# Optimization experiments

Measured on AMD Instinct MI355X. Metric: run time of the kernel, lower is better.

The kernel has to match this reference:

```python
import jax, jax.numpy as jnp
import numpy as np

N_NODES = 100000
N_EDGES = 3200000
IN_DIM = 62
OUT_DIM = 16
EDGE_DIM = 2


def setup_inputs() -> dict:
    key = jax.random.key(0)
    ks = jax.random.split(key, 8)
    h = jax.random.normal(ks[0], (N_NODES, IN_DIM), dtype=jnp.float32)
    e = jax.random.normal(ks[1], (N_EDGES, EDGE_DIM), dtype=jnp.float32)
    src = jax.random.randint(ks[2], (N_EDGES,), 0, N_NODES, dtype=jnp.int32)
    dst = jax.random.randint(ks[3], (N_EDGES,), 0, N_NODES, dtype=jnp.int32)
    # xavier-normal-ish scaled weights
    W_fc = jax.random.normal(ks[4], (OUT_DIM, IN_DIM), dtype=jnp.float32) * 0.2
    W_attn = jax.random.normal(ks[5], (1, 2 * OUT_DIM + EDGE_DIM), dtype=jnp.float32) * 0.2
    W_edge = jax.random.normal(ks[6], (EDGE_DIM, EDGE_DIM), dtype=jnp.float32) * 0.5
    W_e2n = jax.random.normal(ks[7], (OUT_DIM, EDGE_DIM), dtype=jnp.float32) * 0.5
    return {"h": h, "e": e, "src": src, "dst": dst, "W_fc": W_fc,
            "W_attn": W_attn, "W_edge": W_edge, "W_e2n": W_e2n}


def _agat_forward(h, e, src, dst, W_fc, W_attn, W_edge, W_e2n):
    n = h.shape[0]
    d = W_fc.shape[0]
    z = h @ W_fc.T                      # [N, D]
    ex = e @ W_edge.T                   # [E, edge_dim]
    # attn_fc([z_src, z_dst, ex]) split into per-part projections
    Wa_src = W_attn[:, :d]              # [1, D]
    Wa_dst = W_attn[:, d:2 * d]         # [1, D]
    Wa_e = W_attn[:, 2 * d:]            # [1, edge_dim]
    a_src = (z @ Wa_src.T)[:, 0]        # [N] per-node, gathered per-edge
    a_dst = (z @ Wa_dst.T)[:, 0]        # [N]
    a = a_src[src] + a_dst[dst] + (ex @ Wa_e.T)[:, 0]   # [E]
    e_att = jax.nn.leaky_relu(a, negative_slope=0.01)    # [E]
    # segment softmax over incoming edges of each dst node
    m = jax.ops.segment_max(e_att, dst, num_segments=n)  # [N]
    w = jnp.exp(e_att - m[dst])                           # [E]
    denom = jax.ops.segment_sum(w, dst, num_segments=n)   # [N]
    attn = w / denom[dst]                                  # [E]
    # message = z_src + ez; aggregated as attn-weighted sum (matches
    # sum(attn*z) + sum(attn*ez) in reduce_func)
    ez = ex @ W_e2n.T                                      # [E, D]
    msg = attn[:, None] * (z[src] + ez)                    # [E, D]
    return jax.ops.segment_sum(msg, dst, num_segments=n)   # [N, D]


def reference(h, e, src, dst, W_fc, W_attn, W_edge, W_e2n):
    return _agat_forward(h, e, src, dst, W_fc, W_attn, W_edge, W_e2n)
```

## Files before the change

### kernel.cpp

```cpp
#include <hip/hip_runtime.h>
#include <hip/hip_fp16.h>

#define N_NODES 100000
#define N_EDGES 3200000
#define IN_DIM  62
#define OUT_DIM 16

#define EBC    6144
#define EPT    (EBC / 1024)
#define NEB    ((N_EDGES + EBC - 1) / EBC)
#define NPB    ((N_NODES + 1023) / 1024)
#define NBUCK  ((N_NODES + 63) / 64)
#define CAPL   4096
#define CSTR   16

typedef int nat_i2 __attribute__((ext_vector_type(2)));

__global__ __launch_bounds__(1024) void proj_append_kernel(
    const float* __restrict__ h,
    const float* __restrict__ W_fc,
    const float* __restrict__ W_attn,
    const float* __restrict__ e,
    const int*   __restrict__ src,
    const int*   __restrict__ dst,
    __half* __restrict__ zh,
    float* __restrict__ a_src_arr,
    float* __restrict__ a_dst_arr,
    int*   __restrict__ cursor,
    nat_i2* __restrict__ records,
    int cap)
{
    __shared__ int  cnt[NBUCK];
    __shared__ int  pfx[NBUCK];
    __shared__ int  combo[NBUCK];
    __shared__ int2 pay[EBC];
    __shared__ unsigned short pbkt[EBC];
    __shared__ int  wsum[16];

    int tid = threadIdx.x;

    if (blockIdx.x < NPB) {
        int i = blockIdx.x * 1024 + tid;
        if (i >= N_NODES) return;

        float acc[OUT_DIM];
#pragma unroll
        for (int j = 0; j < OUT_DIM; ++j) acc[j] = 0.f;

        const float2* __restrict__ hr = (const float2*)(h + (size_t)i * IN_DIM);
#pragma unroll
        for (int kk = 0; kk < IN_DIM / 2; ++kk) {
            float2 hv = hr[kk];
#pragma unroll
            for (int j = 0; j < OUT_DIM; ++j) {
                acc[j] += hv.x * W_fc[j * IN_DIM + 2 * kk]
                        + hv.y * W_fc[j * IN_DIM + 2 * kk + 1];
            }
        }

        float asrc = 0.f, adst = 0.f;
#pragma unroll
        for (int j = 0; j < OUT_DIM; ++j) {
            asrc += acc[j] * W_attn[j];
            adst += acc[j] * W_attn[OUT_DIM + j];
        }

        union { __half hx[16]; uint4 q[2]; } u;
#pragma unroll
        for (int j = 0; j < OUT_DIM; ++j) u.hx[j] = __float2half(acc[j]);
        uint4* __restrict__ zrow = (uint4*)(zh + (size_t)i * OUT_DIM);
        zrow[0] = u.q[0];
        zrow[1] = u.q[1];

        a_src_arr[i] = asrc;
        a_dst_arr[i] = adst;
        return;
    }

    int be = blockIdx.x - NPB;
    long ebase = (long)be * EBC;
    int chunk_n = (int)min((long)EBC, (long)N_EDGES - ebase);

    int dv[EPT], sv[EPT];
    float2 ev[EPT];
#pragma unroll
    for (int j = 0; j < EPT; ++j) {
        int p = tid + j * 1024;
        dv[j] = -1;
        if (p < chunk_n) {
            long eid = ebase + p;
            dv[j] = dst[eid];
            sv[j] = src[eid];
            ev[j] = ((const float2*)e)[eid];
        }
    }

    for (int t = tid; t < NBUCK; t += 1024) cnt[t] = 0;
    __syncthreads();

#pragma unroll
    for (int j = 0; j < EPT; ++j)
        if (dv[j] >= 0) atomicAdd(&cnt[dv[j] >> 6], 1);
    __syncthreads();

    int b0 = 2 * tid, b1 = b0 + 1;
    int c0 = (b0 < NBUCK) ? cnt[b0] : 0;
    int c1 = (b1 < NBUCK) ? cnt[b1] : 0;
    if (b0 < NBUCK) cnt[b0] = 0;
    if (b1 < NBUCK) cnt[b1] = 0;
    int gb0 = 0, gb1 = 0;
    if (c0) gb0 = atomicAdd(&cursor[b0 * CSTR], c0);
    if (c1) gb1 = atomicAdd(&cursor[b1 * CSTR], c1);

    int ts = c0 + c1;
    {
        int lane = tid & 63, wid = tid >> 6;
        int x = ts;
#pragma unroll
        for (int off = 1; off < 64; off <<= 1) {
            int y = __shfl_up(x, off, 64);
            if (lane >= off) x += y;
        }
        if (lane == 63) wsum[wid] = x;
        __syncthreads();
        if (wid == 0) {
            int v = (lane < 16) ? wsum[lane] : 0;
#pragma unroll
            for (int off = 1; off < 16; off <<= 1) {
                int y = __shfl_up(v, off, 64);
                if (lane >= off) v += y;
            }
            if (lane < 16) wsum[lane] = v;
        }
        __syncthreads();
        int texcl = x - ts + (wid ? wsum[wid - 1] : 0);
        if (b0 < NBUCK) { pfx[b0] = texcl;      combo[b0] = b0 * cap + gb0 - texcl; }
        if (b1 < NBUCK) { pfx[b1] = texcl + c0; combo[b1] = b1 * cap + gb1 - (texcl + c0); }
    }
    __syncthreads();

#pragma unroll
    for (int j = 0; j < EPT; ++j) {
        if (dv[j] >= 0) {
            int b = dv[j] >> 6;
            union { __half2 h2; int i; } uu;
            uu.h2.x = __float2half(ev[j].x);
            uu.h2.y = __float2half(ev[j].y);
            int r = atomicAdd(&cnt[b], 1);
            int q = pfx[b] + r;
            pay[q]  = make_int2(uu.i, sv[j] | ((dv[j] & 63) << 17));
            pbkt[q] = (unsigned short)b;
        }
    }
    __syncthreads();

    for (int p = tid; p < chunk_n; p += 1024) {
        int2 v = pay[p];
        int bb = pbkt[p];
        int pos = combo[bb] + p;
        if (pos < (bb + 1) * cap) {
            nat_i2 vv; vv.x = v.x; vv.y = v.y;
            __builtin_nontemporal_store(vv, records + pos);
        }
    }
}

__global__ __launch_bounds__(1024) void bucket_gather_kernel(
    const int*    __restrict__ cursor,
    const nat_i2* __restrict__ records,
    const __half* __restrict__ zh,
    const float*  __restrict__ a_src_arr,
    const float*  __restrict__ a_dst_arr,
    const float*  __restrict__ W_attn,
    const float*  __restrict__ W_edge,
    const float*  __restrict__ W_e2n,
    float* __restrict__ out, int cap)
{
    __shared__ int2 rec[CAPL];
    __shared__ unsigned short inv[CAPL];
    __shared__ unsigned int exb[CAPL];
    __shared__ int hist[64], pfx[64], cur[64];
    __shared__ float adst_l[64];

    int b   = blockIdx.x;
    int tid = threadIdx.x;
    long lo = (long)b * cap;
    int n   = cursor[b * CSTR];
    int nl  = n < cap ? n : cap;
    if (nl > CAPL) nl = CAPL;

    if (tid < 64) {
        hist[tid] = 0; cur[tid] = 0;
        int node = (b << 6) + tid;
        adst_l[tid] = (node < N_NODES) ? a_dst_arr[node] : 0.f;
    }
    __syncthreads();

    float we00 = W_edge[0], we01 = W_edge[1], we10 = W_edge[2], we11 = W_edge[3];
    float wa0  = W_attn[2 * OUT_DIM], wa1 = W_attn[2 * OUT_DIM + 1];

    int ld0 = -1, ld1 = -1, ld2 = -1, ld3 = -1;
#define EDGEW(J, LD)                                                        \
    {                                                                       \
        int k = tid + (J) * 1024;                                           \
        if (k < nl) {                                                       \
            nat_i2 r = __builtin_nontemporal_load(records + lo + k);        \
            int s  = r.y & 0x1FFFF;                                         \
            LD     = (r.y >> 17) & 63;                                      \
            union { int i; __half2 h2; } ue; ue.i = r.x;                    \
            float e0 = __low2float(ue.h2), e1 = __high2float(ue.h2);        \
            float ex0 = e0 * we00 + e1 * we01;                              \
            float ex1 = e0 * we10 + e1 * we11;                              \
            float a = a_src_arr[s] + adst_l[LD] + ex0 * wa0 + ex1 * wa1;    \
            float ea = (a > 0.f) ? a : 0.01f * a;                           \
            float w  = __expf(ea);                                          \
            rec[k] = make_int2(__float_as_int(w), r.y);                     \
            union { unsigned int i; __half2 h2; } up;                       \
            up.h2.x = __float2half(ex0);                                    \
            up.h2.y = __float2half(ex1);                                    \
            exb[k] = up.i;                                                  \
            atomicAdd(&hist[LD], 1);                                        \
        }                                                                   \
    }
    EDGEW(0, ld0) EDGEW(1, ld1) EDGEW(2, ld2) EDGEW(3, ld3)
#undef EDGEW
    __syncthreads();

    if (tid < 64) pfx[tid] = hist[tid];
    __syncthreads();
    for (int off = 1; off < 64; off <<= 1) {
        int t = 0;
        if (tid < 64 && tid >= off) t = pfx[tid - off];
        __syncthreads();
        if (tid < 64) pfx[tid] += t;
        __syncthreads();
    }
    if (tid < 64) pfx[tid] -= hist[tid];
    __syncthreads();

#define INVW(J, LD)                                                         \
    if (LD >= 0) {                                                          \
        int k = tid + (J) * 1024;                                           \
        int r = atomicAdd(&cur[LD], 1);                                     \
        inv[pfx[LD] + r] = (unsigned short)k;                               \
    }
    INVW(0, ld0) INVW(1, ld1) INVW(2, ld2) INVW(3, ld3)
#undef INVW
    __syncthreads();

    int ld   = tid >> 4;
    int lane = tid & 15;
    int node = (b << 6) + ld;
    if (node >= N_NODES) return;

    int m    = hist[ld];
    int base = pfx[ld];

    float acc0 = 0.f, acc1 = 0.f, accw0 = 0.f, accw1 = 0.f;
    float ax00 = 0.f, ax01 = 0.f, ax10 = 0.f, ax11 = 0.f;

    int i = 0;
    for (; i + 1 < m; i += 2) {
        int k0 = inv[base + i];
        int k1 = inv[base + i + 1];
        int2 r0 = rec[k0];
        int2 r1 = rec[k1];
        float w0 = __int_as_float(r0.x);
        float w1 = __int_as_float(r1.x);
        int s0 = r0.y & 0x1FFFF;
        int s1 = r1.y & 0x1FFFF;
        union { unsigned int i; __half2 h2; } x0, x1;
        x0.i = exb[k0];
        x1.i = exb[k1];

        float zv0 = __half2float(zh[s0 * OUT_DIM + lane]);
        float zv1 = __half2float(zh[s1 * OUT_DIM + lane]);

        acc0  += w0 * zv0;                 acc1  += w1 * zv1;
        accw0 += w0;                       accw1 += w1;
        ax00  += w0 * __low2float(x0.h2);  ax01  += w1 * __low2float(x1.h2);
        ax10  += w0 * __high2float(x0.h2); ax11  += w1 * __high2float(x1.h2);
    }
    if (i < m) {
        int k0 = inv[base + i];
        int2 r0 = rec[k0];
        float w0 = __int_as_float(r0.x);
        int s0 = r0.y & 0x1FFFF;
        union { unsigned int i; __half2 h2; } x0;
        x0.i = exb[k0];
        float zv0 = __half2float(zh[s0 * OUT_DIM + lane]);
        acc0  += w0 * zv0;
        accw0 += w0;
        ax00  += w0 * __low2float(x0.h2);
        ax10  += w0 * __high2float(x0.h2);
    }

    float acc  = acc0 + acc1;
    float accw = accw0 + accw1;
    float ax0  = ax00 + ax01;
    float ax1  = ax10 + ax11;

    float ez   = ax0 * W_e2n[2 * lane] + ax1 * W_e2n[2 * lane + 1];
    float invw = (accw != 0.f) ? (1.f / accw) : 0.f;
    out[(size_t)node * OUT_DIM + lane] = (acc + ez) * invw;
}


__global__ __launch_bounds__(256) void node_proj_fb_kernel(
    const float* __restrict__ h,
    const float* __restrict__ W_fc,
    const float* __restrict__ W_attn,
    float* __restrict__ z,
    float* __restrict__ a_src_arr,
    float* __restrict__ a_dst_arr,
    float* __restrict__ denom,
    float* __restrict__ out)
{
    int i = blockIdx.x * blockDim.x + threadIdx.x;
    if (i >= N_NODES) return;

    float acc[OUT_DIM];
#pragma unroll
    for (int j = 0; j < OUT_DIM; ++j) acc[j] = 0.f;

    const float2* __restrict__ hr = (const float2*)(h + (size_t)i * IN_DIM);
#pragma unroll
    for (int kk = 0; kk < IN_DIM / 2; ++kk) {
        float2 hv = hr[kk];
#pragma unroll
        for (int j = 0; j < OUT_DIM; ++j) {
            acc[j] += hv.x * W_fc[j * IN_DIM + 2 * kk]
                    + hv.y * W_fc[j * IN_DIM + 2 * kk + 1];
        }
    }

    float asrc = 0.f, adst = 0.f;
#pragma unroll
    for (int j = 0; j < OUT_DIM; ++j) {
        asrc += acc[j] * W_attn[j];
        adst += acc[j] * W_attn[OUT_DIM + j];
    }

    float4* __restrict__ zrow = (float4*)(z + (size_t)i * OUT_DIM);
    zrow[0] = make_float4(acc[0],  acc[1],  acc[2],  acc[3]);
    zrow[1] = make_float4(acc[4],  acc[5],  acc[6],  acc[7]);
    zrow[2] = make_float4(acc[8],  acc[9],  acc[10], acc[11]);
    zrow[3] = make_float4(acc[12], acc[13], acc[14], acc[15]);

    a_src_arr[i] = asrc;
    a_dst_arr[i] = adst;
    denom[i] = 0.f;

    float4 z4 = make_float4(0.f, 0.f, 0.f, 0.f);
    float4* __restrict__ orow = (float4*)(out + (size_t)i * OUT_DIM);
    orow[0] = z4; orow[1] = z4; orow[2] = z4; orow[3] = z4;
}

__global__ __launch_bounds__(256) void edge_kernel(
    const float* __restrict__ e,
    const int*   __restrict__ src,
    const int*   __restrict__ dst,
    const float* __restrict__ W_attn,
    const float* __restrict__ W_edge,
    const float* __restrict__ W_e2n,
    const float* __restrict__ z,
    const float* __restrict__ a_src_arr,
    const float* __restrict__ a_dst_arr,
    float* __restrict__ denom,
    float* __restrict__ out)
{
    int eid = blockIdx.x * blockDim.x + threadIdx.x;
    if (eid >= N_EDGES) return;

    int s = src[eid];
    int d = dst[eid];

    float2 ev = ((const float2*)e)[eid];
    float ex0 = ev.x * W_edge[0] + ev.y * W_edge[1];
    float ex1 = ev.x * W_edge[2] + ev.y * W_edge[3];

    float a = a_src_arr[s] + a_dst_arr[d]
            + ex0 * W_attn[2 * OUT_DIM] + ex1 * W_attn[2 * OUT_DIM + 1];
    float ea = (a > 0.f) ? a : 0.01f * a;
    float w  = __expf(ea);

    unsafeAtomicAdd(denom + d, w);

    const float4* __restrict__ zrow = (const float4*)(z + (size_t)s * OUT_DIM);
    float4 z0 = zrow[0], z1 = zrow[1], z2 = zrow[2], z3 = zrow[3];

    float* __restrict__ orow = out + (size_t)d * OUT_DIM;
    float zs[OUT_DIM] = { z0.x, z0.y, z0.z, z0.w,
                          z1.x, z1.y, z1.z, z1.w,
                          z2.x, z2.y, z2.z, z2.w,
                          z3.x, z3.y, z3.z, z3.w };
#pragma unroll
    for (int j = 0; j < OUT_DIM; ++j) {
        float ez = ex0 * W_e2n[2 * j] + ex1 * W_e2n[2 * j + 1];
        unsafeAtomicAdd(orow + j, w * (zs[j] + ez));
    }
}

__global__ __launch_bounds__(256) void normalize_kernel(
    float* __restrict__ out, const float* __restrict__ denom)
{
    int tid = blockIdx.x * blockDim.x + threadIdx.x;
    const int total = N_NODES * OUT_DIM / 4;
    if (tid >= total) return;
    int n = tid >> 2;
    float dn = denom[n];
    float inv = (dn != 0.f) ? (1.f / dn) : 0.f;
    float4 v = ((float4*)out)[tid];
    v.x *= inv; v.y *= inv; v.z *= inv; v.w *= inv;
    ((float4*)out)[tid] = v;
}

extern "C" void kernel_launch(void* const* d_in, const int* in_sizes, int n_in,
                              void* d_out, int out_size, void* d_ws, size_t ws_size,
                              hipStream_t stream)
{
    const float* h      = (const float*)d_in[0];
    const float* e      = (const float*)d_in[1];
    const int*   src    = (const int*)  d_in[2];
    const int*   dst    = (const int*)  d_in[3];
    const float* W_fc   = (const float*)d_in[4];
    const float* W_attn = (const float*)d_in[5];
    const float* W_edge = (const float*)d_in[6];
    const float* W_e2n  = (const float*)d_in[7];
    float* out = (float*)d_out;

    char* ws = (char*)d_ws;

    size_t off = 0;
    __half* zh        = (__half*)(ws + off); off += (size_t)N_NODES * OUT_DIM * 2;
    float*  a_src_arr = (float*) (ws + off); off += (size_t)N_NODES * 4;
    float*  a_dst_arr = (float*) (ws + off); off += (size_t)N_NODES * 4;
    int*    cursor    = (int*)   (ws + off); off += (size_t)NBUCK * CSTR * 4;
    size_t rec_off = (off + 255) & ~(size_t)255;

    int cap = 0;
    if      (ws_size >= rec_off + (size_t)NBUCK * 4096 * 8) cap = 4096;
    else if (ws_size >= rec_off + (size_t)NBUCK * 3072 * 8) cap = 3072;
    else if (ws_size >= rec_off + (size_t)NBUCK * 2560 * 8) cap = 2560;
    else if (ws_size >= rec_off + (size_t)NBUCK * 2304 * 8) cap = 2304;

    if (cap) {
        nat_i2* records = (nat_i2*)(ws + rec_off);

        hipMemsetAsync(cursor, 0, (size_t)NBUCK * CSTR * sizeof(int), stream);

        proj_append_kernel<<<NPB + NEB, 1024, 0, stream>>>(
            h, W_fc, W_attn, e, src, dst,
            zh, a_src_arr, a_dst_arr, cursor, records, cap);

        bucket_gather_kernel<<<NBUCK, 1024, 0, stream>>>(
            cursor, records, zh, a_src_arr, a_dst_arr,
            W_attn, W_edge, W_e2n, out, cap);
    } else {
        size_t foff = 0;
        float* z     = (float*)(ws + foff); foff += (size_t)N_NODES * OUT_DIM * 4;
        float* asrc  = (float*)(ws + foff); foff += (size_t)N_NODES * 4;
        float* adst  = (float*)(ws + foff); foff += (size_t)N_NODES * 4;
        float* denom = (float*)(ws + foff); foff += (size_t)N_NODES * 4;

        node_proj_fb_kernel<<<(N_NODES + 255) / 256, 256, 0, stream>>>(
            h, W_fc, W_attn, z, asrc, adst, denom, out);

        edge_kernel<<<(N_EDGES + 255) / 256, 256, 0, stream>>>(
            e, src, dst, W_attn, W_edge, W_e2n, z, asrc, adst, denom, out);

        normalize_kernel<<<(N_NODES * OUT_DIM / 4 + 255) / 256, 256, 0, stream>>>(
            out, denom);
    }
}
```

Before: 220.5 us.

## Use 256-node buckets with chunked two-block gather and atomic partial accumulation

Buckets grow from 64 to 256 destination nodes, and each bucket's record segment is padded to a multiple of 8 with zero-weight sentinel records. This is meant to give aligned, fuller writes and fewer cursor atomics. The gather kernel now runs two 512-thread blocks per bucket. They walk 2048-record chunks alternately, compute per-node partial numerators and denominators with 4 lanes per node using 8-byte loads of z, and add them atomically into zeroed global buffers. A separate normalize kernel then divides. This removes the fixed per-bucket shared-memory capacity, but adds atomics, an extra pass, and a larger memset.

```diff
diff --git a/kernel.cpp b/kernel.cpp
--- a/kernel.cpp
+++ b/kernel.cpp
@@ -6,13 +6,17 @@
 #define IN_DIM  62
 #define OUT_DIM 16
 
-#define EBC    6144
-#define EPT    (EBC / 1024)
+#define EBC    4096
+#define EPT    4
 #define NEB    ((N_EDGES + EBC - 1) / EBC)
 #define NPB    ((N_NODES + 1023) / 1024)
-#define NBUCK  ((N_NODES + 63) / 64)
-#define CAPL   4096
+#define BSH    8
+#define BNODES 256
+#define NB2    ((N_NODES + BNODES - 1) / BNODES)
+#define PCAP   6912
+#define CHK    2048
 #define CSTR   16
+#define PADY   ((int)0x82000000u)
 
 typedef int nat_i2 __attribute__((ext_vector_type(2)));
 
@@ -30,12 +34,13 @@
     nat_i2* __restrict__ records,
     int cap)
 {
-    __shared__ int  cnt[NBUCK];
-    __shared__ int  pfx[NBUCK];
-    __shared__ int  combo[NBUCK];
-    __shared__ int2 pay[EBC];
-    __shared__ unsigned short pbkt[EBC];
+    __shared__ int  cnt[NB2];
+    __shared__ int  pfx[NB2];
+    __shared__ int  combo[NB2];
+    __shared__ int2 pay[PCAP];
+    __shared__ unsigned short pbkt[PCAP];
     __shared__ int  wsum[16];
+    __shared__ int  sh_ptot;
 
     int tid = threadIdx.x;
 
@@ -95,27 +100,26 @@
         }
     }
 
-    for (int t = tid; t < NBUCK; t += 1024) cnt[t] = 0;
+    for (int t = tid; t < NB2; t += 1024) cnt[t] = 0;
     __syncthreads();
 
 #pragma unroll
     for (int j = 0; j < EPT; ++j)
-        if (dv[j] >= 0) atomicAdd(&cnt[dv[j] >> 6], 1);
+        if (dv[j] >= 0) atomicAdd(&cnt[dv[j] >> BSH], 1);
     __syncthreads();
 
-    int b0 = 2 * tid, b1 = b0 + 1;
-    int c0 = (b0 < NBUCK) ? cnt[b0] : 0;
-    int c1 = (b1 < NBUCK) ? cnt[b1] : 0;
-    if (b0 < NBUCK) cnt[b0] = 0;
-    if (b1 < NBUCK) cnt[b1] = 0;
-    int gb0 = 0, gb1 = 0;
-    if (c0) gb0 = atomicAdd(&cursor[b0 * CSTR], c0);
-    if (c1) gb1 = atomicAdd(&cursor[b1 * CSTR], c1);
-
-    int ts = c0 + c1;
+    int c = 0, n8 = 0, gb = 0;
+    if (tid < NB2) {
+        c  = cnt[tid];
+        n8 = (c + 7) & ~7;
+        cnt[tid] = 0;
+        if (n8) gb = atomicAdd(&cursor[tid * CSTR], n8);
+    }
+
+    int texcl;
     {
         int lane = tid & 63, wid = tid >> 6;
-        int x = ts;
+        int x = n8;
 #pragma unroll
         for (int off = 1; off < 64; off <<= 1) {
             int y = __shfl_up(x, off, 64);
@@ -133,30 +137,38 @@
             if (lane < 16) wsum[lane] = v;
         }
         __syncthreads();
-        int texcl = x - ts + (wid ? wsum[wid - 1] : 0);
-        if (b0 < NBUCK) { pfx[b0] = texcl;      combo[b0] = b0 * cap + gb0 - texcl; }
-        if (b1 < NBUCK) { pfx[b1] = texcl + c0; combo[b1] = b1 * cap + gb1 - (texcl + c0); }
-    }
+        texcl = x - n8 + (wid ? wsum[wid - 1] : 0);
+    }
+
+    if (tid < NB2) {
+        pfx[tid]   = texcl;
+        combo[tid] = tid * cap + gb - texcl;
+        for (int q = texcl; q < texcl + n8; ++q) {
+            pay[q]  = make_int2(0, PADY);
+            pbkt[q] = (unsigned short)tid;
+        }
+    }
+    if (tid == NB2 - 1) sh_ptot = texcl + n8;
     __syncthreads();
 
 #pragma unroll
     for (int j = 0; j < EPT; ++j) {
         if (dv[j] >= 0) {
-            int b = dv[j] >> 6;
+            int b = dv[j] >> BSH;
             union { __half2 h2; int i; } uu;
             uu.h2.x = __float2half(ev[j].x);
             uu.h2.y = __float2half(ev[j].y);
             int r = atomicAdd(&cnt[b], 1);
             int q = pfx[b] + r;
-            pay[q]  = make_int2(uu.i, sv[j] | ((dv[j] & 63) << 17));
-            pbkt[q] = (unsigned short)b;
+            pay[q] = make_int2(uu.i, sv[j] | ((dv[j] & (BNODES - 1)) << 17));
         }
     }
     __syncthreads();
 
-    for (int p = tid; p < chunk_n; p += 1024) {
-        int2 v = pay[p];
-        int bb = pbkt[p];
+    int ptot = sh_ptot;
+    for (int p = tid; p < ptot; p += 1024) {
+        int2 v  = pay[p];
+        int  bb = pbkt[p];
         int pos = combo[bb] + p;
         if (pos < (bb + 1) * cap) {
             nat_i2 vv; vv.x = v.x; vv.y = v.y;
@@ -165,7 +177,7 @@
     }
 }
 
-__global__ __launch_bounds__(1024) void bucket_gather_kernel(
+__global__ __launch_bounds__(512) void bucket_gather_kernel(
     const int*    __restrict__ cursor,
     const nat_i2* __restrict__ records,
     const __half* __restrict__ zh,
@@ -174,24 +186,26 @@
     const float*  __restrict__ W_attn,
     const float*  __restrict__ W_edge,
     const float*  __restrict__ W_e2n,
-    float* __restrict__ out, int cap)
-{
-    __shared__ int2 rec[CAPL];
-    __shared__ unsigned short inv[CAPL];
-    __shared__ unsigned int exb[CAPL];
-    __shared__ int hist[64], pfx[64], cur[64];
-    __shared__ float adst_l[64];
-
-    int b   = blockIdx.x;
+    float* __restrict__ num,
+    float* __restrict__ den,
+    int cap)
+{
+    __shared__ int2 rec[CHK];
+    __shared__ unsigned int exb[CHK];
+    __shared__ unsigned short inv[CHK];
+    __shared__ int hist[257], pfxs[257], cur[257];
+    __shared__ float adst_l[BNODES];
+    __shared__ int wsum4[4];
+
+    int b   = blockIdx.x >> 1;
+    int hb  = blockIdx.x & 1;
     int tid = threadIdx.x;
     long lo = (long)b * cap;
     int n   = cursor[b * CSTR];
-    int nl  = n < cap ? n : cap;
-    if (nl > CAPL) nl = CAPL;
-
-    if (tid < 64) {
-        hist[tid] = 0; cur[tid] = 0;
-        int node = (b << 6) + tid;
+    if (n > cap) n = cap;
+
+    if (tid < BNODES) {
+        int node = b * BNODES + tid;
         adst_l[tid] = (node < N_NODES) ? a_dst_arr[node] : 0.f;
     }
     __syncthreads();
@@ -199,110 +213,138 @@
     float we00 = W_edge[0], we01 = W_edge[1], we10 = W_edge[2], we11 = W_edge[3];
     float wa0  = W_attn[2 * OUT_DIM], wa1 = W_attn[2 * OUT_DIM + 1];
 
-    int ld0 = -1, ld1 = -1, ld2 = -1, ld3 = -1;
+    int lane4 = (tid & 3) * 4;
+
+    float aA[2][4], aW[2], aX0[2], aX1[2];
+#pragma unroll
+    for (int sp = 0; sp < 2; ++sp) {
+        aW[sp] = 0.f; aX0[sp] = 0.f; aX1[sp] = 0.f;
+#pragma unroll
+        for (int f = 0; f < 4; ++f) aA[sp][f] = 0.f;
+    }
+
+    for (int cb = hb * CHK; cb < n; cb += 2 * CHK) {
+        int cn = n - cb; if (cn > CHK) cn = CHK;
+
+        __syncthreads();
+        if (tid < 257) { hist[tid] = 0; cur[tid] = 0; }
+        __syncthreads();
+
+        int ld0 = -1, ld1 = -1, ld2 = -1, ld3 = -1;
 #define EDGEW(J, LD)                                                        \
-    {                                                                       \
-        int k = tid + (J) * 1024;                                           \
-        if (k < nl) {                                                       \
-            nat_i2 r = __builtin_nontemporal_load(records + lo + k);        \
-            int s  = r.y & 0x1FFFF;                                         \
-            LD     = (r.y >> 17) & 63;                                      \
-            union { int i; __half2 h2; } ue; ue.i = r.x;                    \
-            float e0 = __low2float(ue.h2), e1 = __high2float(ue.h2);        \
-            float ex0 = e0 * we00 + e1 * we01;                              \
-            float ex1 = e0 * we10 + e1 * we11;                              \
-            float a = a_src_arr[s] + adst_l[LD] + ex0 * wa0 + ex1 * wa1;    \
-            float ea = (a > 0.f) ? a : 0.01f * a;                           \
-            float w  = __expf(ea);                                          \
-            rec[k] = make_int2(__float_as_int(w), r.y);                     \
-            union { unsigned int i; __half2 h2; } up;                       \
-            up.h2.x = __float2half(ex0);                                    \
-            up.h2.y = __float2half(ex1);                                    \
-            exb[k] = up.i;                                                  \
-            atomicAdd(&hist[LD], 1);                                        \
-        }                                                                   \
-    }
-    EDGEW(0, ld0) EDGEW(1, ld1) EDGEW(2, ld2) EDGEW(3, ld3)
+        {                                                                   \
+            int kk = tid + (J) * 512;                                       \
+            if (kk < cn) {                                                  \
+                nat_i2 r = __builtin_nontemporal_load(records + lo + cb + kk); \
+                int s = r.y & 0x1FFFF;                                      \
+                LD = (r.y >> 17) & 0x1FF;                  \
+                union { int i; __half2 h2; } ue; ue.i = r.x;                \
+                float e0 = __low2float(ue.h2), e1 = __high2float(ue.h2);    \
+                float ex0 = e0 * we00 + e1 * we01;                          \
+                float ex1 = e0 * we10 + e1 * we11;                          \
+                float a = a_src_arr[s] + adst_l[LD & 255] + ex0 * wa0 + ex1 * wa1; \
+                float ea = (a > 0.f) ? a : 0.01f * a;                       \
+                float w  = __expf(ea);                                      \
+                if (r.y < 0) w = 0.f;                       \
+                rec[kk] = make_int2(__float_as_int(w), r.y);                \
+                union { unsigned int i; __half2 h2; } up;                   \
+                up.h2.x = __float2half(ex0);                                \
+                up.h2.y = __float2half(ex1);                                \
+                exb[kk] = up.i;                                             \
+                atomicAdd(&hist[LD], 1);                                    \
+            }                                                               \
+        }
+        EDGEW(0, ld0) EDGEW(1, ld1) EDGEW(2, ld2) EDGEW(3, ld3)
 #undef EDGEW
-    __syncthreads();
-
-    if (tid < 64) pfx[tid] = hist[tid];
-    __syncthreads();
-    for (int off = 1; off < 64; off <<= 1) {
-        int t = 0;
-        if (tid < 64 && tid >= off) t = pfx[tid - off];
-        __syncthreads();
-        if (tid < 64) pfx[tid] += t;
-        __syncthreads();
-    }
-    if (tid < 64) pfx[tid] -= hist[tid];
-    __syncthreads();
+        __syncthreads();
+
+        int hh = 0, xx = 0;
+        int lane = tid & 63, wv = tid >> 6;
+        if (tid < 256) {
+            hh = hist[tid]; xx = hh;
+#pragma unroll
+            for (int off = 1; off < 64; off <<= 1) {
+                int y = __shfl_up(xx, off, 64);
+                if (lane >= off) xx += y;
+            }
+            if (lane == 63) wsum4[wv] = xx;
+        }
+        __syncthreads();
+        if (tid == 0) {
+            int rr = 0;
+#pragma unroll
+            for (int i2 = 0; i2 < 4; ++i2) { int t = wsum4[i2]; wsum4[i2] = rr; rr += t; }
+        }
+        __syncthreads();
+        if (tid < 256) {
+            pfxs[tid] = xx - hh + wsum4[wv];
+            if (tid == 255) pfxs[256] = xx + wsum4[3];
+        }
+        __syncthreads();
 
 #define INVW(J, LD)                                                         \
-    if (LD >= 0) {                                                          \
-        int k = tid + (J) * 1024;                                           \
-        int r = atomicAdd(&cur[LD], 1);                                     \
-        inv[pfx[LD] + r] = (unsigned short)k;                               \
-    }
-    INVW(0, ld0) INVW(1, ld1) INVW(2, ld2) INVW(3, ld3)
+        if (LD >= 0) {                                                      \
+            int kk = tid + (J) * 512;                                       \
+            int r = atomicAdd(&cur[LD], 1);                                 \
+            inv[pfxs[LD] + r] = (unsigned short)kk;                         \
+        }
+        INVW(0, ld0) INVW(1, ld1) INVW(2, ld2) INVW(3, ld3)
 #undef INVW
-    __syncthreads();
-
-    int ld   = tid >> 4;
-    int lane = tid & 15;
-    int node = (b << 6) + ld;
-    if (node >= N_NODES) return;
-
-    int m    = hist[ld];
-    int base = pfx[ld];
-
-    float acc0 = 0.f, acc1 = 0.f, accw0 = 0.f, accw1 = 0.f;
-    float ax00 = 0.f, ax01 = 0.f, ax10 = 0.f, ax11 = 0.f;
-
-    int i = 0;
-    for (; i + 1 < m; i += 2) {
-        int k0 = inv[base + i];
-        int k1 = inv[base + i + 1];
-        int2 r0 = rec[k0];
-        int2 r1 = rec[k1];
-        float w0 = __int_as_float(r0.x);
-        float w1 = __int_as_float(r1.x);
-        int s0 = r0.y & 0x1FFFF;
-        int s1 = r1.y & 0x1FFFF;
-        union { unsigned int i; __half2 h2; } x0, x1;
-        x0.i = exb[k0];
-        x1.i = exb[k1];
-
-        float zv0 = __half2float(zh[s0 * OUT_DIM + lane]);
-        float zv1 = __half2float(zh[s1 * OUT_DIM + lane]);
-
-        acc0  += w0 * zv0;                 acc1  += w1 * zv1;
-        accw0 += w0;                       accw1 += w1;
-        ax00  += w0 * __low2float(x0.h2);  ax01  += w1 * __low2float(x1.h2);
-        ax10  += w0 * __high2float(x0.h2); ax11  += w1 * __high2float(x1.h2);
-    }
-    if (i < m) {
-        int k0 = inv[base + i];
-        int2 r0 = rec[k0];
-        float w0 = __int_as_float(r0.x);
-        int s0 = r0.y & 0x1FFFF;
-        union { unsigned int i; __half2 h2; } x0;
-        x0.i = exb[k0];
-        float zv0 = __half2float(zh[s0 * OUT_DIM + lane]);
-        acc0  += w0 * zv0;
-        accw0 += w0;
-        ax00  += w0 * __low2float(x0.h2);
-        ax10  += w0 * __high2float(x0.h2);
-    }
-
-    float acc  = acc0 + acc1;
-    float accw = accw0 + accw1;
-    float ax0  = ax00 + ax01;
-    float ax1  = ax10 + ax11;
-
-    float ez   = ax0 * W_e2n[2 * lane] + ax1 * W_e2n[2 * lane + 1];
-    float invw = (accw != 0.f) ? (1.f / accw) : 0.f;
-    out[(size_t)node * OUT_DIM + lane] = (acc + ez) * invw;
+        __syncthreads();
+
+#pragma unroll
+        for (int sp = 0; sp < 2; ++sp) {
+            int nl_  = sp * 128 + (tid >> 2);
+            int m    = hist[nl_];
+            int base = pfxs[nl_];
+            for (int i = 0; i < m; ++i) {
+                int k = inv[base + i];
+                int2 r = rec[k];
+                float w = __int_as_float(r.x);
+                int s = r.y & 0x1FFFF;
+                unsigned int xe = exb[k];
+                uint2 zz = *(const uint2*)(zh + (size_t)s * OUT_DIM + lane4);
+                union { unsigned int i; __half2 h2; } za, zb, xu;
+                za.i = zz.x; zb.i = zz.y; xu.i = xe;
+                aA[sp][0] += w * __low2float(za.h2);
+                aA[sp][1] += w * __high2float(za.h2);
+                aA[sp][2] += w * __low2float(zb.h2);
+                aA[sp][3] += w * __high2float(zb.h2);
+                aW[sp]  += w;
+                aX0[sp] += w * __low2float(xu.h2);
+                aX1[sp] += w * __high2float(xu.h2);
+            }
+        }
+    }
+
+#pragma unroll
+    for (int sp = 0; sp < 2; ++sp) {
+        int node = b * BNODES + sp * 128 + (tid >> 2);
+        if (node < N_NODES) {
+#pragma unroll
+            for (int f = 0; f < 4; ++f) {
+                int j = lane4 + f;
+                float ez = aX0[sp] * W_e2n[2 * j] + aX1[sp] * W_e2n[2 * j + 1];
+                unsafeAtomicAdd(&num[(size_t)node * OUT_DIM + j], aA[sp][f] + ez);
+            }
+            if ((tid & 3) == 0) unsafeAtomicAdd(&den[node], aW[sp]);
+        }
+    }
+}
+
+__global__ __launch_bounds__(256) void normalize2_kernel(
+    const float* __restrict__ num, const float* __restrict__ den,
+    float* __restrict__ out)
+{
+    int t = blockIdx.x * blockDim.x + threadIdx.x;
+    const int total = N_NODES * OUT_DIM / 4;
+    if (t >= total) return;
+    int node = t >> 2;
+    float dn = den[node];
+    float iv = (dn != 0.f) ? (1.f / dn) : 0.f;
+    float4 v = ((const float4*)num)[t];
+    v.x *= iv; v.y *= iv; v.z *= iv; v.w *= iv;
+    ((float4*)out)[t] = v;
 }
 
 
@@ -435,27 +477,33 @@
     __half* zh        = (__half*)(ws + off); off += (size_t)N_NODES * OUT_DIM * 2;
     float*  a_src_arr = (float*) (ws + off); off += (size_t)N_NODES * 4;
     float*  a_dst_arr = (float*) (ws + off); off += (size_t)N_NODES * 4;
-    int*    cursor    = (int*)   (ws + off); off += (size_t)NBUCK * CSTR * 4;
+    off = (off + 255) & ~(size_t)255;
+    size_t mz_off = off;
+    int*    cursor = (int*)(ws + off);  off += ((size_t)NB2 * CSTR * 4 + 255) & ~(size_t)255;
+    float*  num    = (float*)(ws + off); off += (size_t)N_NODES * OUT_DIM * 4;
+    float*  den    = (float*)(ws + off); off += (size_t)N_NODES * 4;
+    size_t mz_bytes = off - mz_off;
     size_t rec_off = (off + 255) & ~(size_t)255;
 
     int cap = 0;
-    if      (ws_size >= rec_off + (size_t)NBUCK * 4096 * 8) cap = 4096;
-    else if (ws_size >= rec_off + (size_t)NBUCK * 3072 * 8) cap = 3072;
-    else if (ws_size >= rec_off + (size_t)NBUCK * 2560 * 8) cap = 2560;
-    else if (ws_size >= rec_off + (size_t)NBUCK * 2304 * 8) cap = 2304;
+    if      (ws_size >= rec_off + (size_t)NB2 * 12288 * 8) cap = 12288;
+    else if (ws_size >= rec_off + (size_t)NB2 * 11776 * 8) cap = 11776;
 
     if (cap) {
         nat_i2* records = (nat_i2*)(ws + rec_off);
 
-        hipMemsetAsync(cursor, 0, (size_t)NBUCK * CSTR * sizeof(int), stream);
+        hipMemsetAsync(ws + mz_off, 0, mz_bytes, stream);
 
         proj_append_kernel<<<NPB + NEB, 1024, 0, stream>>>(
             h, W_fc, W_attn, e, src, dst,
             zh, a_src_arr, a_dst_arr, cursor, records, cap);
 
-        bucket_gather_kernel<<<NBUCK, 1024, 0, stream>>>(
+        bucket_gather_kernel<<<2 * NB2, 512, 0, stream>>>(
             cursor, records, zh, a_src_arr, a_dst_arr,
-            W_attn, W_edge, W_e2n, out, cap);
+            W_attn, W_edge, W_e2n, num, den, cap);
+
+        normalize2_kernel<<<(N_NODES * OUT_DIM / 4 + 255) / 256, 256, 0, stream>>>(
+            num, den, out);
     } else {
         size_t foff = 0;
         float* z     = (float*)(ws + foff); foff += (size_t)N_NODES * OUT_DIM * 4;
```

After: 234.1 us. +6.2%, slower.

## Fuse projection, append and gather into one persistent cooperative kernel

Applied to the files above, without the earlier changes.

Replaces the memset plus two kernel launches with a single cooperative persistent kernel. It zeroes the cursors, runs the projection and append work units in a grid-stride loop, then the per-bucket gather, with grid-wide syncs between phases. Shared memory is a union of the two phase layouts, and the edge chunk shrinks from 6144 to 4096 so the persistent blocks fit. This removes launch gaps and kernel boundaries, but it adds grid-sync cost, limits the grid to one or two blocks per CU, and risks load imbalance.

```diff
diff --git a/kernel.cpp b/kernel.cpp
--- a/kernel.cpp
+++ b/kernel.cpp
@@ -1,83 +1,93 @@
 #include <hip/hip_runtime.h>
 #include <hip/hip_fp16.h>
+#include <hip/hip_cooperative_groups.h>
+
+namespace cg = cooperative_groups;
 
 #define N_NODES 100000
 #define N_EDGES 3200000
 #define IN_DIM  62
 #define OUT_DIM 16
 
-#define EBC    6144
-#define EPT    (EBC / 1024)
+#define EBC    4096
+#define EPT    4
 #define NEB    ((N_EDGES + EBC - 1) / EBC)
 #define NPB    ((N_NODES + 1023) / 1024)
 #define NBUCK  ((N_NODES + 63) / 64)
 #define CAPL   4096
 #define CSTR   16
+#define NCU    256
 
 typedef int nat_i2 __attribute__((ext_vector_type(2)));
 
-__global__ __launch_bounds__(1024) void proj_append_kernel(
-    const float* __restrict__ h,
-    const float* __restrict__ W_fc,
+struct AppendSh {
+    int  cnt[NBUCK];
+    int  pfx[NBUCK];
+    int  combo[NBUCK];
+    int2 pay[EBC];
+    unsigned short pbkt[EBC];
+    int  wsum[16];
+};
+struct GatherSh {
+    int2 rec[CAPL];
+    unsigned short inv[CAPL];
+    unsigned int exb[CAPL];
+    int hist[64], pfx[64], cur[64];
+    float adst_l[64];
+};
+union ShArena { AppendSh a; GatherSh g; };
+
+__device__ __forceinline__ void do_proj(
+    int u, int tid,
+    const float* __restrict__ h, const float* __restrict__ W_fc,
     const float* __restrict__ W_attn,
-    const float* __restrict__ e,
-    const int*   __restrict__ src,
-    const int*   __restrict__ dst,
-    __half* __restrict__ zh,
-    float* __restrict__ a_src_arr,
-    float* __restrict__ a_dst_arr,
-    int*   __restrict__ cursor,
-    nat_i2* __restrict__ records,
-    int cap)
-{
-    __shared__ int  cnt[NBUCK];
-    __shared__ int  pfx[NBUCK];
-    __shared__ int  combo[NBUCK];
-    __shared__ int2 pay[EBC];
-    __shared__ unsigned short pbkt[EBC];
-    __shared__ int  wsum[16];
-
-    int tid = threadIdx.x;
-
-    if (blockIdx.x < NPB) {
-        int i = blockIdx.x * 1024 + tid;
-        if (i >= N_NODES) return;
-
-        float acc[OUT_DIM];
-#pragma unroll
-        for (int j = 0; j < OUT_DIM; ++j) acc[j] = 0.f;
-
-        const float2* __restrict__ hr = (const float2*)(h + (size_t)i * IN_DIM);
-#pragma unroll
-        for (int kk = 0; kk < IN_DIM / 2; ++kk) {
-            float2 hv = hr[kk];
-#pragma unroll
-            for (int j = 0; j < OUT_DIM; ++j) {
-                acc[j] += hv.x * W_fc[j * IN_DIM + 2 * kk]
-                        + hv.y * W_fc[j * IN_DIM + 2 * kk + 1];
-            }
-        }
-
-        float asrc = 0.f, adst = 0.f;
+    __half* __restrict__ zh, float* __restrict__ a_src_arr,
+    float* __restrict__ a_dst_arr)
+{
+    int i = u * 1024 + tid;
+    if (i >= N_NODES) return;
+
+    float acc[OUT_DIM];
+#pragma unroll
+    for (int j = 0; j < OUT_DIM; ++j) acc[j] = 0.f;
+
+    const float2* __restrict__ hr = (const float2*)(h + (size_t)i * IN_DIM);
+#pragma unroll
+    for (int kk = 0; kk < IN_DIM / 2; ++kk) {
+        float2 hv = hr[kk];
 #pragma unroll
         for (int j = 0; j < OUT_DIM; ++j) {
-            asrc += acc[j] * W_attn[j];
-            adst += acc[j] * W_attn[OUT_DIM + j];
-        }
-
-        union { __half hx[16]; uint4 q[2]; } u;
-#pragma unroll
-        for (int j = 0; j < OUT_DIM; ++j) u.hx[j] = __float2half(acc[j]);
-        uint4* __restrict__ zrow = (uint4*)(zh + (size_t)i * OUT_DIM);
-        zrow[0] = u.q[0];
-        zrow[1] = u.q[1];
-
-        a_src_arr[i] = asrc;
-        a_dst_arr[i] = adst;
-        return;
-    }
-
-    int be = blockIdx.x - NPB;
+            acc[j] += hv.x * W_fc[j * IN_DIM + 2 * kk]
+                    + hv.y * W_fc[j * IN_DIM + 2 * kk + 1];
+        }
+    }
+
+    float asrc = 0.f, adst = 0.f;
+#pragma unroll
+    for (int j = 0; j < OUT_DIM; ++j) {
+        asrc += acc[j] * W_attn[j];
+        adst += acc[j] * W_attn[OUT_DIM + j];
+    }
+
+    union { __half hx[16]; uint4 q[2]; } uq;
+#pragma unroll
+    for (int j = 0; j < OUT_DIM; ++j) uq.hx[j] = __float2half(acc[j]);
+    uint4* __restrict__ zrow = (uint4*)(zh + (size_t)i * OUT_DIM);
+    zrow[0] = uq.q[0];
+    zrow[1] = uq.q[1];
+
+    a_src_arr[i] = asrc;
+    a_dst_arr[i] = adst;
+}
+
+__device__ __forceinline__ void do_append(
+    int be, int tid, AppendSh& S,
+    const float* __restrict__ e, const int* __restrict__ src,
+    const int* __restrict__ dst, int* __restrict__ cursor,
+    nat_i2* __restrict__ records, int cap)
+{
+    __syncthreads();
+
     long ebase = (long)be * EBC;
     int chunk_n = (int)min((long)EBC, (long)N_EDGES - ebase);
 
@@ -95,19 +105,19 @@
         }
     }
 
-    for (int t = tid; t < NBUCK; t += 1024) cnt[t] = 0;
+    for (int t = tid; t < NBUCK; t += 1024) S.cnt[t] = 0;
     __syncthreads();
 
 #pragma unroll
     for (int j = 0; j < EPT; ++j)
-        if (dv[j] >= 0) atomicAdd(&cnt[dv[j] >> 6], 1);
+        if (dv[j] >= 0) atomicAdd(&S.cnt[dv[j] >> 6], 1);
     __syncthreads();
 
     int b0 = 2 * tid, b1 = b0 + 1;
-    int c0 = (b0 < NBUCK) ? cnt[b0] : 0;
-    int c1 = (b1 < NBUCK) ? cnt[b1] : 0;
-    if (b0 < NBUCK) cnt[b0] = 0;
-    if (b1 < NBUCK) cnt[b1] = 0;
+    int c0 = (b0 < NBUCK) ? S.cnt[b0] : 0;
+    int c1 = (b1 < NBUCK) ? S.cnt[b1] : 0;
+    if (b0 < NBUCK) S.cnt[b0] = 0;
+    if (b1 < NBUCK) S.cnt[b1] = 0;
     int gb0 = 0, gb1 = 0;
     if (c0) gb0 = atomicAdd(&cursor[b0 * CSTR], c0);
     if (c1) gb1 = atomicAdd(&cursor[b1 * CSTR], c1);
@@ -121,21 +131,21 @@
             int y = __shfl_up(x, off, 64);
             if (lane >= off) x += y;
         }
-        if (lane == 63) wsum[wid] = x;
+        if (lane == 63) S.wsum[wid] = x;
         __syncthreads();
         if (wid == 0) {
-            int v = (lane < 16) ? wsum[lane] : 0;
+            int v = (lane < 16) ? S.wsum[lane] : 0;
 #pragma unroll
             for (int off = 1; off < 16; off <<= 1) {
                 int y = __shfl_up(v, off, 64);
                 if (lane >= off) v += y;
             }
-            if (lane < 16) wsum[lane] = v;
+            if (lane < 16) S.wsum[lane] = v;
         }
         __syncthreads();
-        int texcl = x - ts + (wid ? wsum[wid - 1] : 0);
-        if (b0 < NBUCK) { pfx[b0] = texcl;      combo[b0] = b0 * cap + gb0 - texcl; }
-        if (b1 < NBUCK) { pfx[b1] = texcl + c0; combo[b1] = b1 * cap + gb1 - (texcl + c0); }
+        int texcl = x - ts + (wid ? S.wsum[wid - 1] : 0);
+        if (b0 < NBUCK) { S.pfx[b0] = texcl;      S.combo[b0] = b0 * cap + gb0 - texcl; }
+        if (b1 < NBUCK) { S.pfx[b1] = texcl + c0; S.combo[b1] = b1 * cap + gb1 - (texcl + c0); }
     }
     __syncthreads();
 
@@ -146,18 +156,18 @@
             union { __half2 h2; int i; } uu;
             uu.h2.x = __float2half(ev[j].x);
             uu.h2.y = __float2half(ev[j].y);
-            int r = atomicAdd(&cnt[b], 1);
-            int q = pfx[b] + r;
-            pay[q]  = make_int2(uu.i, sv[j] | ((dv[j] & 63) << 17));
-            pbkt[q] = (unsigned short)b;
+            int r = atomicAdd(&S.cnt[b], 1);
+            int q = S.pfx[b] + r;
+            S.pay[q]  = make_int2(uu.i, sv[j] | ((dv[j] & 63) << 17));
+            S.pbkt[q] = (unsigned short)b;
         }
     }
     __syncthreads();
 
     for (int p = tid; p < chunk_n; p += 1024) {
-        int2 v = pay[p];
-        int bb = pbkt[p];
-        int pos = combo[bb] + p;
+        int2 v  = S.pay[p];
+        int  bb = S.pbkt[p];
+        int pos = S.combo[bb] + p;
         if (pos < (bb + 1) * cap) {
             nat_i2 vv; vv.x = v.x; vv.y = v.y;
             __builtin_nontemporal_store(vv, records + pos);
@@ -165,34 +175,24 @@
     }
 }
 
-__global__ __launch_bounds__(1024) void bucket_gather_kernel(
-    const int*    __restrict__ cursor,
-    const nat_i2* __restrict__ records,
-    const __half* __restrict__ zh,
-    const float*  __restrict__ a_src_arr,
-    const float*  __restrict__ a_dst_arr,
-    const float*  __restrict__ W_attn,
-    const float*  __restrict__ W_edge,
-    const float*  __restrict__ W_e2n,
+__device__ __forceinline__ void do_gather(
+    int b, int tid, GatherSh& S,
+    const int* __restrict__ cursor, const nat_i2* __restrict__ records,
+    const __half* __restrict__ zh, const float* __restrict__ a_src_arr,
+    const float* __restrict__ a_dst_arr, const float* __restrict__ W_attn,
+    const float* __restrict__ W_edge, const float* __restrict__ W_e2n,
     float* __restrict__ out, int cap)
 {
-    __shared__ int2 rec[CAPL];
-    __shared__ unsigned short inv[CAPL];
-    __shared__ unsigned int exb[CAPL];
-    __shared__ int hist[64], pfx[64], cur[64];
-    __shared__ float adst_l[64];
-
-    int b   = blockIdx.x;
-    int tid = threadIdx.x;
+    __syncthreads();
+
     long lo = (long)b * cap;
     int n   = cursor[b * CSTR];
     int nl  = n < cap ? n : cap;
-    if (nl > CAPL) nl = CAPL;
 
     if (tid < 64) {
-        hist[tid] = 0; cur[tid] = 0;
+        S.hist[tid] = 0; S.cur[tid] = 0;
         int node = (b << 6) + tid;
-        adst_l[tid] = (node < N_NODES) ? a_dst_arr[node] : 0.f;
+        S.adst_l[tid] = (node < N_NODES) ? a_dst_arr[node] : 0.f;
     }
     __syncthreads();
 
@@ -211,38 +211,38 @@
             float e0 = __low2float(ue.h2), e1 = __high2float(ue.h2);        \
             float ex0 = e0 * we00 + e1 * we01;                              \
             float ex1 = e0 * we10 + e1 * we11;                              \
-            float a = a_src_arr[s] + adst_l[LD] + ex0 * wa0 + ex1 * wa1;    \
+            float a = a_src_arr[s] + S.adst_l[LD] + ex0 * wa0 + ex1 * wa1;  \
             float ea = (a > 0.f) ? a : 0.01f * a;                           \
             float w  = __expf(ea);                                          \
-            rec[k] = make_int2(__float_as_int(w), r.y);                     \
+            S.rec[k] = make_int2(__float_as_int(w), r.y);                   \
             union { unsigned int i; __half2 h2; } up;                       \
             up.h2.x = __float2half(ex0);                                    \
             up.h2.y = __float2half(ex1);                                    \
-            exb[k] = up.i;                                                  \
-            atomicAdd(&hist[LD], 1);                                        \
+            S.exb[k] = up.i;                                                \
+            atomicAdd(&S.hist[LD], 1);                                      \
         }                                                                   \
     }
     EDGEW(0, ld0) EDGEW(1, ld1) EDGEW(2, ld2) EDGEW(3, ld3)
 #undef EDGEW
     __syncthreads();
 
-    if (tid < 64) pfx[tid] = hist[tid];
+    if (tid < 64) S.pfx[tid] = S.hist[tid];
     __syncthreads();
     for (int off = 1; off < 64; off <<= 1) {
         int t = 0;
-        if (tid < 64 && tid >= off) t = pfx[tid - off];
+        if (tid < 64 && tid >= off) t = S.pfx[tid - off];
         __syncthreads();
-        if (tid < 64) pfx[tid] += t;
+        if (tid < 64) S.pfx[tid] += t;
         __syncthreads();
     }
-    if (tid < 64) pfx[tid] -= hist[tid];
+    if (tid < 64) S.pfx[tid] -= S.hist[tid];
     __syncthreads();
 
 #define INVW(J, LD)                                                         \
     if (LD >= 0) {                                                          \
         int k = tid + (J) * 1024;                                           \
-        int r = atomicAdd(&cur[LD], 1);                                     \
-        inv[pfx[LD] + r] = (unsigned short)k;                               \
+        int r = atomicAdd(&S.cur[LD], 1);                                   \
+        S.inv[S.pfx[LD] + r] = (unsigned short)k;                           \
     }
     INVW(0, ld0) INVW(1, ld1) INVW(2, ld2) INVW(3, ld3)
 #undef INVW
@@ -251,27 +251,26 @@
     int ld   = tid >> 4;
     int lane = tid & 15;
     int node = (b << 6) + ld;
-    if (node >= N_NODES) return;
-
-    int m    = hist[ld];
-    int base = pfx[ld];
+
+    int m    = S.hist[ld];
+    int base = S.pfx[ld];
 
     float acc0 = 0.f, acc1 = 0.f, accw0 = 0.f, accw1 = 0.f;
     float ax00 = 0.f, ax01 = 0.f, ax10 = 0.f, ax11 = 0.f;
 
     int i = 0;
     for (; i + 1 < m; i += 2) {
-        int k0 = inv[base + i];
-        int k1 = inv[base + i + 1];
-        int2 r0 = rec[k0];
-        int2 r1 = rec[k1];
+        int k0 = S.inv[base + i];
+        int k1 = S.inv[base + i + 1];
+        int2 r0 = S.rec[k0];
+        int2 r1 = S.rec[k1];
         float w0 = __int_as_float(r0.x);
         float w1 = __int_as_float(r1.x);
         int s0 = r0.y & 0x1FFFF;
         int s1 = r1.y & 0x1FFFF;
         union { unsigned int i; __half2 h2; } x0, x1;
-        x0.i = exb[k0];
-        x1.i = exb[k1];
+        x0.i = S.exb[k0];
+        x1.i = S.exb[k1];
 
         float zv0 = __half2float(zh[s0 * OUT_DIM + lane]);
         float zv1 = __half2float(zh[s1 * OUT_DIM + lane]);
@@ -282,12 +281,12 @@
         ax10  += w0 * __high2float(x0.h2); ax11  += w1 * __high2float(x1.h2);
     }
     if (i < m) {
-        int k0 = inv[base + i];
-        int2 r0 = rec[k0];
+        int k0 = S.inv[base + i];
+        int2 r0 = S.rec[k0];
         float w0 = __int_as_float(r0.x);
         int s0 = r0.y & 0x1FFFF;
         union { unsigned int i; __half2 h2; } x0;
-        x0.i = exb[k0];
+        x0.i = S.exb[k0];
         float zv0 = __half2float(zh[s0 * OUT_DIM + lane]);
         acc0  += w0 * zv0;
         accw0 += w0;
@@ -295,14 +294,71 @@
         ax10  += w0 * __high2float(x0.h2);
     }
 
-    float acc  = acc0 + acc1;
-    float accw = accw0 + accw1;
-    float ax0  = ax00 + ax01;
-    float ax1  = ax10 + ax11;
-
-    float ez   = ax0 * W_e2n[2 * lane] + ax1 * W_e2n[2 * lane + 1];
-    float invw = (accw != 0.f) ? (1.f / accw) : 0.f;
-    out[(size_t)node * OUT_DIM + lane] = (acc + ez) * invw;
+    if (node < N_NODES) {
+        float acc  = acc0 + acc1;
+        float accw = accw0 + accw1;
+        float ax0  = ax00 + ax01;
+        float ax1  = ax10 + ax11;
+
+        float ez   = ax0 * W_e2n[2 * lane] + ax1 * W_e2n[2 * lane + 1];
+        float invw = (accw != 0.f) ? (1.f / accw) : 0.f;
+        out[(size_t)node * OUT_DIM + lane] = (acc + ez) * invw;
+    }
+}
+
+__global__ __launch_bounds__(1024) void fused_kernel(
+    const float* __restrict__ h, const float* __restrict__ e,
+    const int* __restrict__ src, const int* __restrict__ dst,
+    const float* __restrict__ W_fc, const float* __restrict__ W_attn,
+    const float* __restrict__ W_edge, const float* __restrict__ W_e2n,
+    __half* __restrict__ zh, float* __restrict__ a_src_arr,
+    float* __restrict__ a_dst_arr, int* __restrict__ cursor,
+    nat_i2* __restrict__ records, float* __restrict__ out, int cap)
+{
+    __shared__ ShArena sh;
+    cg::grid_group grid = cg::this_grid();
+    int tid = threadIdx.x;
+
+    for (int t = blockIdx.x * 1024 + tid; t < NBUCK * CSTR; t += gridDim.x * 1024)
+        cursor[t] = 0;
+    grid.sync();
+
+    for (int u = blockIdx.x; u < NPB + NEB; u += gridDim.x) {
+        if (u < NPB) do_proj(u, tid, h, W_fc, W_attn, zh, a_src_arr, a_dst_arr);
+        else         do_append(u - NPB, tid, sh.a, e, src, dst, cursor, records, cap);
+    }
+    grid.sync();
+
+    for (int b = blockIdx.x; b < NBUCK; b += gridDim.x)
+        do_gather(b, tid, sh.g, cursor, records, zh, a_src_arr, a_dst_arr,
+                  W_attn, W_edge, W_e2n, out, cap);
+}
+
+__global__ __launch_bounds__(1024) void proj_append_kernel(
+    const float* __restrict__ h, const float* __restrict__ W_fc,
+    const float* __restrict__ W_attn, const float* __restrict__ e,
+    const int* __restrict__ src, const int* __restrict__ dst,
+    __half* __restrict__ zh, float* __restrict__ a_src_arr,
+    float* __restrict__ a_dst_arr, int* __restrict__ cursor,
+    nat_i2* __restrict__ records, int cap)
+{
+    __shared__ AppendSh sh;
+    if (blockIdx.x < NPB)
+        do_proj(blockIdx.x, threadIdx.x, h, W_fc, W_attn, zh, a_src_arr, a_dst_arr);
+    else
+        do_append(blockIdx.x - NPB, threadIdx.x, sh, e, src, dst, cursor, records, cap);
+}
+
+__global__ __launch_bounds__(1024) void bucket_gather_kernel(
+    const int* __restrict__ cursor, const nat_i2* __restrict__ records,
+    const __half* __restrict__ zh, const float* __restrict__ a_src_arr,
+    const float* __restrict__ a_dst_arr, const float* __restrict__ W_attn,
+    const float* __restrict__ W_edge, const float* __restrict__ W_e2n,
+    float* __restrict__ out, int cap)
+{
+    __shared__ GatherSh sh;
+    do_gather(blockIdx.x, threadIdx.x, sh, cursor, records, zh,
+              a_src_arr, a_dst_arr, W_attn, W_edge, W_e2n, out, cap);
 }
 
 
@@ -435,7 +491,10 @@
     __half* zh        = (__half*)(ws + off); off += (size_t)N_NODES * OUT_DIM * 2;
     float*  a_src_arr = (float*) (ws + off); off += (size_t)N_NODES * 4;
     float*  a_dst_arr = (float*) (ws + off); off += (size_t)N_NODES * 4;
-    int*    cursor    = (int*)   (ws + off); off += (size_t)NBUCK * CSTR * 4;
+    off = (off + 255) & ~(size_t)255;
+    int*    cursor = (int*)(ws + off);
+    size_t  cur_bytes = (size_t)NBUCK * CSTR * 4;
+    off += (cur_bytes + 255) & ~(size_t)255;
     size_t rec_off = (off + 255) & ~(size_t)255;
 
     int cap = 0;
@@ -447,15 +506,33 @@
     if (cap) {
         nat_i2* records = (nat_i2*)(ws + rec_off);
 
-        hipMemsetAsync(cursor, 0, (size_t)NBUCK * CSTR * sizeof(int), stream);
-
-        proj_append_kernel<<<NPB + NEB, 1024, 0, stream>>>(
-            h, W_fc, W_attn, e, src, dst,
-            zh, a_src_arr, a_dst_arr, cursor, records, cap);
-
-        bucket_gather_kernel<<<NBUCK, 1024, 0, stream>>>(
-            cursor, records, zh, a_src_arr, a_dst_arr,
-            W_attn, W_edge, W_e2n, out, cap);
+        hipError_t lerr = hipErrorUnknown;
+        int maxB = 0;
+        hipError_t qerr = hipOccupancyMaxActiveBlocksPerMultiprocessor(
+            &maxB, reinterpret_cast<const void*>(fused_kernel), 1024, 0);
+        if (qerr == hipSuccess && maxB > 0) {
+            int gridB = (maxB >= 2 ? 2 : 1) * NCU;
+            void* kargs[] = {
+                (void*)&h, (void*)&e, (void*)&src, (void*)&dst,
+                (void*)&W_fc, (void*)&W_attn, (void*)&W_edge, (void*)&W_e2n,
+                (void*)&zh, (void*)&a_src_arr, (void*)&a_dst_arr,
+                (void*)&cursor, (void*)&records, (void*)&out, (void*)&cap };
+            lerr = hipLaunchCooperativeKernel(
+                reinterpret_cast<const void*>(fused_kernel),
+                dim3(gridB), dim3(1024), kargs, 0, stream);
+        }
+
+        if (lerr != hipSuccess) {
+            hipMemsetAsync(cursor, 0, cur_bytes, stream);
+
+            proj_append_kernel<<<NPB + NEB, 1024, 0, stream>>>(
+                h, W_fc, W_attn, e, src, dst,
+                zh, a_src_arr, a_dst_arr, cursor, records, cap);
+
+            bucket_gather_kernel<<<NBUCK, 1024, 0, stream>>>(
+                cursor, records, zh, a_src_arr, a_dst_arr,
+                W_attn, W_edge, W_e2n, out, cap);
+        }
     } else {
         size_t foff = 0;
         float* z     = (float*)(ws + foff); foff += (size_t)N_NODES * OUT_DIM * 4;
```

Measured after the change: 240.0 us. 1.09x slower.
